# Kernel optimization log

Measured on AMD Instinct MI355X. Metric: run time of the kernel, lower is better.

The kernel has to match this reference:

```python
import jax, jax.numpy as jnp
import numpy as np


def setup_inputs() -> dict:
    key = jax.random.key(0)
    ks = jax.random.split(key, 8)
    B, C, H, W = 4, 128, 64, 64
    C8 = C // 8
    return {
        "x": jax.random.normal(ks[0], (B, C, H, W), dtype=jnp.float32),
        "Wq": jax.random.normal(ks[1], (C8, C), dtype=jnp.float32) * (1.0 / np.sqrt(C)),
        "bq": jax.random.normal(ks[2], (C8,), dtype=jnp.float32) * 0.01,
        "Wk": jax.random.normal(ks[3], (C8, C), dtype=jnp.float32) * (1.0 / np.sqrt(C)),
        "bk": jax.random.normal(ks[4], (C8,), dtype=jnp.float32) * 0.01,
        "Wv": jax.random.normal(ks[5], (C, C), dtype=jnp.float32) * (1.0 / np.sqrt(C)),
        "bv": jax.random.normal(ks[6], (C,), dtype=jnp.float32) * 0.01,
        "gamma": jax.random.normal(ks[7], (1,), dtype=jnp.float32),
    }


def reference(x, Wq, bq, Wk, bk, Wv, bv, gamma):
    B, C, H, W = x.shape
    N = H * W
    xf = x.reshape(B, C, N)  # flatten spatial dims; 1x1 conv == channel matmul
    q = jnp.einsum("oc,bcn->bon", Wq, xf) + bq[None, :, None]  # (B, C8, N)
    k = jnp.einsum("oc,bcn->bon", Wk, xf) + bk[None, :, None]  # (B, C8, N)
    v = jnp.einsum("oc,bcn->bon", Wv, xf) + bv[None, :, None]  # (B, C, N)
    scores = jnp.einsum("bci,bcj->bij", q, k)  # (B, N, N), query rows x key cols
    attn = jax.nn.softmax(scores, axis=-1)
    out = jnp.einsum("bcj,bij->bci", v, attn)  # (B, C, N)
    out = out.reshape(B, C, H, W)
    return gamma[0] * out + x
```

## Files before the change

kernel.cpp:

```cpp
#include <hip/hip_runtime.h>
#include <math.h>

typedef __attribute__((ext_vector_type(8))) short bf16x8;
typedef __attribute__((ext_vector_type(16))) float f32x16;

constexpr int Bn = 4, Cn = 128, C8n = 16, Nn = 4096;

#if __has_builtin(__builtin_amdgcn_exp2f)
#define EXP2F(x) __builtin_amdgcn_exp2f(x)
#else
#define EXP2F(x) exp2f(x)
#endif

__device__ inline unsigned short f2bf(float f) {
    unsigned u = __builtin_bit_cast(unsigned, f);
    u += 0x7fff + ((u >> 16) & 1);
    return (unsigned short)(u >> 16);
}
__device__ inline unsigned pack2(float a, float b) {
    return (unsigned)f2bf(a) | ((unsigned)f2bf(b) << 16);
}
__device__ inline unsigned pkt(float a, float b) {
#if __has_builtin(__builtin_amdgcn_perm)
    return __builtin_amdgcn_perm(__builtin_bit_cast(unsigned, b),
                                 __builtin_bit_cast(unsigned, a), 0x07060302u);
#else
    return (__builtin_bit_cast(unsigned, a) >> 16) |
           (__builtin_bit_cast(unsigned, b) & 0xffff0000u);
#endif
}

__global__ __launch_bounds__(256) void qkv_kernel(
    const float* __restrict__ x,
    const float* __restrict__ Wq, const float* __restrict__ bq,
    const float* __restrict__ Wk, const float* __restrict__ bk,
    const float* __restrict__ Wv, const float* __restrict__ bv,
    unsigned short* __restrict__ qT, unsigned short* __restrict__ kT,
    unsigned short* __restrict__ vsw)
{
    __shared__ unsigned short wlds[160 * 128];
    __shared__ unsigned short v_s[32 * 128];
    __shared__ float qk_s[32][65];
    __shared__ float bfl[160];

    const int tid = threadIdx.x;
    const int b = blockIdx.x >> 6, n0 = (blockIdx.x & 63) << 6;
    const int w = tid >> 6, lane = tid & 63, col = lane & 31, half = lane >> 5;
    const float L2E = 1.4426950408889634f;

    {
        unsigned* wl32 = (unsigned*)wlds;
        for (int i = tid; i < 160 * 32; i += 256) {
            int r = i >> 5, cq = (i & 31) << 2;
            const float* src; float sc = 1.0f;
            if (r < 16)      { src = Wq + (size_t)r * Cn;        sc = L2E; }
            else if (r < 32) { src = Wk + (size_t)(r - 16) * Cn; }
            else             { src = Wv + (size_t)(r - 32) * Cn; }
            float4 t = *reinterpret_cast<const float4*>(&src[cq]);
            int G = cq >> 3;
            unsigned* wp = wl32 + 64 * r + 4 * (G ^ (r & 7)) + ((cq & 7) >> 1);
            wp[0] = pack2(t.x * sc, t.y * sc);
            wp[1] = pack2(t.z * sc, t.w * sc);
        }
        if (tid < 160)
            bfl[tid] = (tid < 16) ? bq[tid] * L2E
                     : (tid < 32) ? bk[tid - 16] : bv[tid - 32];
    }

    const int nx = n0 + ((w & 1) << 5);
    const float* xb = x + ((size_t)b * Cn) * Nn + nx + col;
    bf16x8 af[8];
    #pragma unroll
    for (int s = 0; s < 8; ++s) {
        float v[8];
        #pragma unroll
        for (int j = 0; j < 8; ++j)
            v[j] = xb[(size_t)(16 * s + 8 * half + j) * Nn];
        uint4 u = make_uint4(pack2(v[0], v[1]), pack2(v[2], v[3]),
                             pack2(v[4], v[5]), pack2(v[6], v[7]));
        af[s] = __builtin_bit_cast(bf16x8, u);
    }
    __syncthreads();

    const int mb = (w >> 1) ? 3 : 0;
    const bool three = (w >> 1) == 0;
    f32x16 a0, a1, a2;
    {
        float b0 = bfl[32 * mb + col], b1 = bfl[32 * (mb + 1) + col];
        float b2v = three ? bfl[64 + col] : 0.0f;
        #pragma unroll
        for (int r = 0; r < 16; ++r) { a0[r] = b0; a1[r] = b1; a2[r] = b2v; }
    }
    #pragma unroll
    for (int s = 0; s < 8; ++s) {
        const int off = 8 * ((2 * s + half) ^ (col & 7));
        a0 = __builtin_amdgcn_mfma_f32_32x32x16_bf16(af[s],
             *(const bf16x8*)(wlds + 128 * (32 * mb + col) + off), a0, 0, 0, 0);
        a1 = __builtin_amdgcn_mfma_f32_32x32x16_bf16(af[s],
             *(const bf16x8*)(wlds + 128 * (32 * (mb + 1) + col) + off), a1, 0, 0, 0);
        if (three)
            a2 = __builtin_amdgcn_mfma_f32_32x32x16_bf16(af[s],
                 *(const bf16x8*)(wlds + 128 * (64 + col) + off), a2, 0, 0, 0);
    }

    unsigned* vp32 = (unsigned*)v_s;
    #define VS_WRITE(A) { \
        _Pragma("unroll") for (int g = 0; g < 4; ++g) { \
            int n_ = ((w & 1) << 5) + (g << 3) + (half << 2); \
            int Gn = n_ >> 3; \
            int u_ = 64 * col + 4 * (Gn ^ (col & 7)) + (half << 1); \
            vp32[u_]     = pack2(A[4 * g],     A[4 * g + 1]); \
            vp32[u_ + 1] = pack2(A[4 * g + 2], A[4 * g + 3]); } }

    #define VS_OUT(CT) { \
        int c_ = lane & 31, Gt = ((tid >> 6) << 1) + (lane >> 5); \
        bf16x8 fr = *(const bf16x8*)&v_s[128 * c_ + 8 * (Gt ^ (c_ & 7))]; \
        size_t o_ = ((((size_t)b * 256 + (n0 >> 4) + (tid >> 6)) * 4 + (CT)) * 64 + lane) * 8; \
        *reinterpret_cast<uint4*>(&vsw[o_]) = __builtin_bit_cast(uint4, fr); }

    if (w < 2) {
        #pragma unroll
        for (int r = 0; r < 16; ++r)
            qk_s[col][((w & 1) << 5) + (r & 3) + ((r >> 2) << 3) + (half << 2)] = a0[r];
    } else {
        VS_WRITE(a0)
    }
    __syncthreads();
    VS_OUT(2)
    if (tid < 128) {
        int n = tid & 63, which = tid >> 6;
        unsigned wv_[8];
        #pragma unroll
        for (int i = 0; i < 8; ++i)
            wv_[i] = pack2(qk_s[16 * which + 2 * i][n], qk_s[16 * which + 2 * i + 1][n]);
        unsigned short* dst = (which ? kT : qT) + ((size_t)b * Nn + n0 + n) * C8n;
        *reinterpret_cast<uint4*>(dst)     = make_uint4(wv_[0], wv_[1], wv_[2], wv_[3]);
        *reinterpret_cast<uint4*>(dst + 8) = make_uint4(wv_[4], wv_[5], wv_[6], wv_[7]);
    }
    __syncthreads();
    if (w < 2) VS_WRITE(a1)
    __syncthreads();
    VS_OUT(0)
    __syncthreads();
    if (w >= 2) VS_WRITE(a1)
    __syncthreads();
    VS_OUT(3)
    __syncthreads();
    if (w < 2) VS_WRITE(a2)
    __syncthreads();
    VS_OUT(1)
    #undef VS_WRITE
    #undef VS_OUT
}

__global__ __launch_bounds__(512) void attn_kernel(
    const unsigned short* __restrict__ qT, const unsigned short* __restrict__ kT,
    const unsigned short* __restrict__ vsw, const float* __restrict__ x,
    const float* __restrict__ gamma_p, float* __restrict__ out)
{
    __shared__ unsigned sm_u32[8192];
    __shared__ float ls[2][2][64];
    __shared__ float invl[64];

    const int tid = threadIdx.x, wv = tid >> 6, lane = tid & 63;
    const int col = lane & 31, half = lane >> 5;
    const int xcd = blockIdx.x & 7;
    const int b = xcd >> 1;
    const int q0 = ((((blockIdx.x >> 3) << 1) | (xcd & 1))) << 6;

    const unsigned short* qb = qT + (size_t)b * Nn * C8n;
    bf16x8 qf0 = *(const bf16x8*)&qb[(size_t)(q0 + col) * C8n + 8 * half];
    bf16x8 qf1 = *(const bf16x8*)&qb[(size_t)(q0 + 32 + col) * C8n + 8 * half];

    f32x16 accA[4], accB[4];
    #pragma unroll
    for (int ct = 0; ct < 4; ++ct) { accA[ct] = {}; accB[ct] = {}; }
    float l0 = 0.0f, l1 = 0.0f;
    const unsigned short* kb = kT + (size_t)b * Nn * C8n;

    for (int kt = 0; kt < 16; ++kt) {
        const int j0 = (wv << 9) + (kt << 5);
        const size_t vbase = ((((size_t)b * 256 + (j0 >> 4)) * 4) * 64 + lane) * 8;
        bf16x8 va[4], vb2[4];
        #pragma unroll
        for (int ct = 0; ct < 4; ++ct) {
            va[ct]  = *(const bf16x8*)&vsw[vbase + (size_t)ct * 512];
            vb2[ct] = *(const bf16x8*)&vsw[vbase + (size_t)(4 + ct) * 512];
        }
        bf16x8 kf = *(const bf16x8*)&kb[(size_t)(j0 + col) * C8n + 8 * half];
        f32x16 z = {};
        f32x16 s0 = __builtin_amdgcn_mfma_f32_32x32x16_bf16(kf, qf0, z, 0, 0, 0);
        f32x16 s1 = __builtin_amdgcn_mfma_f32_32x32x16_bf16(kf, qf1, z, 0, 0, 0);

        float p0[16], p1[16];
        float ps0 = 0.0f, ps1 = 0.0f;
        #pragma unroll
        for (int r = 0; r < 16; ++r) { p0[r] = EXP2F(s0[r]); ps0 += p0[r]; }
        #pragma unroll
        for (int r = 0; r < 16; ++r) { p1[r] = EXP2F(s1[r]); ps1 += p1[r]; }
        ps0 += __shfl_xor(ps0, 32); l0 += ps0;
        ps1 += __shfl_xor(ps1, 32); l1 += ps1;

        #define MKPF(P, O, F) { \
            unsigned lo0 = pkt(P[O], P[O + 1]), lo1 = pkt(P[O + 2], P[O + 3]); \
            unsigned hi0 = pkt(P[O + 4], P[O + 5]), hi1 = pkt(P[O + 6], P[O + 7]); \
            unsigned t0 = half ? lo0 : hi0, t1 = half ? lo1 : hi1; \
            unsigned r0 = (unsigned)__shfl_xor((int)t0, 32); \
            unsigned r1 = (unsigned)__shfl_xor((int)t1, 32); \
            uint4 u_ = make_uint4(half ? r0 : lo0, half ? r1 : lo1, \
                                  half ? hi0 : r0, half ? hi1 : r1); \
            F = __builtin_bit_cast(bf16x8, u_); }
        bf16x8 pa0, pa1, pb0, pb1;
        MKPF(p0, 0, pa0) MKPF(p0, 8, pa1)
        MKPF(p1, 0, pb0) MKPF(p1, 8, pb1)
        #undef MKPF

        #pragma unroll
        for (int ct = 0; ct < 4; ++ct) {
            accA[ct] = __builtin_amdgcn_mfma_f32_32x32x16_bf16(va[ct],  pa0, accA[ct], 0, 0, 0);
            accA[ct] = __builtin_amdgcn_mfma_f32_32x32x16_bf16(vb2[ct], pa1, accA[ct], 0, 0, 0);
            accB[ct] = __builtin_amdgcn_mfma_f32_32x32x16_bf16(va[ct],  pb0, accB[ct], 0, 0, 0);
            accB[ct] = __builtin_amdgcn_mfma_f32_32x32x16_bf16(vb2[ct], pb1, accB[ct], 0, 0, 0);
        }
    }

    #define SL_STORE(SL) { \
        ls[SL][0][lane] = l0; ls[SL][1][lane] = l1; \
        unsigned* sb = sm_u32 + (SL) * 4096; \
        _Pragma("unroll") for (int ct = 0; ct < 4; ++ct) \
        _Pragma("unroll") for (int i = 0; i < 8; ++i) { \
            sb[((ct) * 8 + i) * 64 + lane]     = pkt(accA[ct][2 * i], accA[ct][2 * i + 1]); \
            sb[((4 + ct) * 8 + i) * 64 + lane] = pkt(accB[ct][2 * i], accB[ct][2 * i + 1]); } }
    #define SL_ADD(SL) { \
        l0 += ls[SL][0][lane]; l1 += ls[SL][1][lane]; \
        unsigned* sb = sm_u32 + (SL) * 4096; \
        _Pragma("unroll") for (int ct = 0; ct < 4; ++ct) \
        _Pragma("unroll") for (int i = 0; i < 8; ++i) { \
            unsigned ua = sb[((ct) * 8 + i) * 64 + lane]; \
            accA[ct][2 * i]     += __builtin_bit_cast(float, ua << 16); \
            accA[ct][2 * i + 1] += __builtin_bit_cast(float, ua & 0xffff0000u); \
            unsigned ub = sb[((4 + ct) * 8 + i) * 64 + lane]; \
            accB[ct][2 * i]     += __builtin_bit_cast(float, ub << 16); \
            accB[ct][2 * i + 1] += __builtin_bit_cast(float, ub & 0xffff0000u); } }
    #define SL_RMW(SL) { \
        ls[SL][0][lane] += l0; ls[SL][1][lane] += l1; \
        unsigned* sb = sm_u32 + (SL) * 4096; \
        _Pragma("unroll") for (int ct = 0; ct < 4; ++ct) \
        _Pragma("unroll") for (int i = 0; i < 8; ++i) { \
            unsigned ua = sb[((ct) * 8 + i) * 64 + lane]; \
            float x0 = __builtin_bit_cast(float, ua << 16) + accA[ct][2 * i]; \
            float x1 = __builtin_bit_cast(float, ua & 0xffff0000u) + accA[ct][2 * i + 1]; \
            sb[((ct) * 8 + i) * 64 + lane] = pkt(x0, x1); \
            unsigned ub = sb[((4 + ct) * 8 + i) * 64 + lane]; \
            float y0 = __builtin_bit_cast(float, ub << 16) + accB[ct][2 * i]; \
            float y1 = __builtin_bit_cast(float, ub & 0xffff0000u) + accB[ct][2 * i + 1]; \
            sb[((4 + ct) * 8 + i) * 64 + lane] = pkt(y0, y1); } }

    if (wv == 4 || wv == 5) SL_STORE(wv - 4)
    __syncthreads();
    if (wv == 0 || wv == 1) SL_ADD(wv)
    __syncthreads();
    if (wv == 6 || wv == 7) SL_STORE(wv - 6)
    __syncthreads();
    if (wv == 2 || wv == 3) SL_RMW(wv - 2)
    __syncthreads();
    if (wv == 0 || wv == 1) SL_ADD(wv)
    __syncthreads();
    if (wv == 1) SL_STORE(0)
    __syncthreads();
    float* sf = (float*)sm_u32;
    if (wv == 0) {
        SL_ADD(0)
        #pragma unroll
        for (int ct = 0; ct < 4; ++ct)
            #pragma unroll
            for (int r = 0; r < 16; ++r) {
                sf[((ct) * 16 + r) * 64 + lane]     = accA[ct][r];
                sf[((4 + ct) * 16 + r) * 64 + lane] = accB[ct][r];
            }
        if (lane < 32) { invl[col] = 1.0f / l0; invl[32 + col] = 1.0f / l1; }
    }
    __syncthreads();
    #undef SL_STORE
    #undef SL_ADD
    #undef SL_RMW

    {
        const float g = gamma_p[0];
        const int n = tid & 63, ci = tid >> 6;
        const float il = invl[n];
        const int qs = n >> 5, nc = n & 31;
        #pragma unroll
        for (int p = 0; p < 16; ++p) {
            int ch = (p << 3) + ci;
            int ct = ch >> 5, chl = ch & 31;
            int h = (chl >> 2) & 1, r = (chl & 3) | ((chl >> 3) << 2);
            float val = sf[((qs * 4 + ct) * 16 + r) * 64 + nc + (h << 5)];
            size_t idx = ((size_t)(b * Cn + ch)) * Nn + q0 + n;
            out[idx] = g * (val * il) + x[idx];
        }
    }
}

extern "C" void kernel_launch(void* const* d_in, const int* in_sizes, int n_in,
                              void* d_out, int out_size, void* d_ws, size_t ws_size,
                              hipStream_t stream)
{
    const float* x     = (const float*)d_in[0];
    const float* Wq    = (const float*)d_in[1];
    const float* bq    = (const float*)d_in[2];
    const float* Wk    = (const float*)d_in[3];
    const float* bk    = (const float*)d_in[4];
    const float* Wv    = (const float*)d_in[5];
    const float* bv    = (const float*)d_in[6];
    const float* gamma = (const float*)d_in[7];
    float* out = (float*)d_out;

    unsigned short* ws16 = (unsigned short*)d_ws;
    unsigned short* qTw  = ws16;
    unsigned short* kTw  = qTw + (size_t)Bn * Nn * C8n;
    unsigned short* vsww = kTw + (size_t)Bn * Nn * C8n;

    qkv_kernel<<<dim3(256), dim3(256), 0, stream>>>(
        x, Wq, bq, Wk, bk, Wv, bv, qTw, kTw, vsww);

    attn_kernel<<<dim3(256), dim3(512), 0, stream>>>(
        qTw, kTw, vsww, x, gamma, out);
}
```

Baseline: 114.1 us.

## Stage full V tile in LDS once and split attention loop by query half

The QKV kernel now holds the whole 128x64 V tile in shared memory, so all waves write their V fragments at once and then each wave stores one channel tile. This replaces the previous sequence of alternating writes, reads and many block barriers. In the attention kernel the two query halves are processed one after the other inside each key step, which shortens the live range of the score and probability arrays and is meant to lower register pressure. The loop is also marked not to unroll. The larger V buffer raises LDS use in the QKV kernel, and the sequential halves may leave less room to overlap MFMA with exp work.

Result: no change. 113.8 us (-0.2%).

```diff
diff --git a/kernel.cpp b/kernel.cpp
--- a/kernel.cpp
+++ b/kernel.cpp
@@ -39,7 +39,7 @@
     unsigned short* __restrict__ vsw)
 {
     __shared__ unsigned short wlds[160 * 128];
-    __shared__ unsigned short v_s[32 * 128];
+    __shared__ unsigned short v_s[128 * 64];
     __shared__ float qk_s[32][65];
     __shared__ float bfl[160];
 
@@ -104,29 +104,27 @@
     }
 
     unsigned* vp32 = (unsigned*)v_s;
-    #define VS_WRITE(A) { \
+    #define VS_WRITE(A, C0) { \
+        const int c_ = (C0) + col; \
         _Pragma("unroll") for (int g = 0; g < 4; ++g) { \
-            int n_ = ((w & 1) << 5) + (g << 3) + (half << 2); \
-            int Gn = n_ >> 3; \
-            int u_ = 64 * col + 4 * (Gn ^ (col & 7)) + (half << 1); \
-            vp32[u_]     = pack2(A[4 * g],     A[4 * g + 1]); \
-            vp32[u_ + 1] = pack2(A[4 * g + 2], A[4 * g + 3]); } }
-
-    #define VS_OUT(CT) { \
-        int c_ = lane & 31, Gt = ((tid >> 6) << 1) + (lane >> 5); \
-        bf16x8 fr = *(const bf16x8*)&v_s[128 * c_ + 8 * (Gt ^ (c_ & 7))]; \
-        size_t o_ = ((((size_t)b * 256 + (n0 >> 4) + (tid >> 6)) * 4 + (CT)) * 64 + lane) * 8; \
-        *reinterpret_cast<uint4*>(&vsw[o_]) = __builtin_bit_cast(uint4, fr); }
+            int Gn = ((w & 1) << 2) + g; \
+            unsigned* up = vp32 + 32 * c_ + 4 * (Gn ^ (c_ & 7)) + (half << 1); \
+            up[0] = pack2(A[4 * g],     A[4 * g + 1]); \
+            up[1] = pack2(A[4 * g + 2], A[4 * g + 3]); } }
 
     if (w < 2) {
         #pragma unroll
         for (int r = 0; r < 16; ++r)
             qk_s[col][((w & 1) << 5) + (r & 3) + ((r >> 2) << 3) + (half << 2)] = a0[r];
+        VS_WRITE(a1, 0)
+        VS_WRITE(a2, 32)
     } else {
-        VS_WRITE(a0)
-    }
-    __syncthreads();
-    VS_OUT(2)
+        VS_WRITE(a0, 64)
+        VS_WRITE(a1, 96)
+    }
+    #undef VS_WRITE
+    __syncthreads();
+
     if (tid < 128) {
         int n = tid & 63, which = tid >> 6;
         unsigned wv_[8];
@@ -137,20 +135,16 @@
         *reinterpret_cast<uint4*>(dst)     = make_uint4(wv_[0], wv_[1], wv_[2], wv_[3]);
         *reinterpret_cast<uint4*>(dst + 8) = make_uint4(wv_[4], wv_[5], wv_[6], wv_[7]);
     }
-    __syncthreads();
-    if (w < 2) VS_WRITE(a1)
-    __syncthreads();
-    VS_OUT(0)
-    __syncthreads();
-    if (w >= 2) VS_WRITE(a1)
-    __syncthreads();
-    VS_OUT(3)
-    __syncthreads();
-    if (w < 2) VS_WRITE(a2)
-    __syncthreads();
-    VS_OUT(1)
-    #undef VS_WRITE
-    #undef VS_OUT
+    {
+        const int ct = w, c_ = (ct << 5) + col;
+        #pragma unroll
+        for (int t = 0; t < 4; ++t) {
+            int Gn = (t << 1) + half;
+            bf16x8 fr = *(const bf16x8*)(vp32 + 32 * c_ + 4 * (Gn ^ (c_ & 7)));
+            size_t o_ = ((((size_t)b * 256 + (n0 >> 4) + t) * 4 + ct) * 64 + lane) * 8;
+            *reinterpret_cast<uint4*>(&vsw[o_]) = __builtin_bit_cast(uint4, fr);
+        }
+    }
 }
 
 __global__ __launch_bounds__(512) void attn_kernel(
@@ -178,6 +172,17 @@
     float l0 = 0.0f, l1 = 0.0f;
     const unsigned short* kb = kT + (size_t)b * Nn * C8n;
 
+    #define MKPF(P, O, F) { \
+        unsigned lo0 = pkt(P[O], P[O + 1]), lo1 = pkt(P[O + 2], P[O + 3]); \
+        unsigned hi0 = pkt(P[O + 4], P[O + 5]), hi1 = pkt(P[O + 6], P[O + 7]); \
+        unsigned t0 = half ? lo0 : hi0, t1 = half ? lo1 : hi1; \
+        unsigned r0 = (unsigned)__shfl_xor((int)t0, 32); \
+        unsigned r1 = (unsigned)__shfl_xor((int)t1, 32); \
+        uint4 u_ = make_uint4(half ? r0 : lo0, half ? r1 : lo1, \
+                              half ? hi0 : r0, half ? hi1 : r1); \
+        F = __builtin_bit_cast(bf16x8, u_); }
+
+    #pragma unroll 1
     for (int kt = 0; kt < 16; ++kt) {
         const int j0 = (wv << 9) + (kt << 5);
         const size_t vbase = ((((size_t)b * 256 + (j0 >> 4)) * 4) * 64 + lane) * 8;
@@ -189,40 +194,37 @@
         }
         bf16x8 kf = *(const bf16x8*)&kb[(size_t)(j0 + col) * C8n + 8 * half];
         f32x16 z = {};
-        f32x16 s0 = __builtin_amdgcn_mfma_f32_32x32x16_bf16(kf, qf0, z, 0, 0, 0);
-        f32x16 s1 = __builtin_amdgcn_mfma_f32_32x32x16_bf16(kf, qf1, z, 0, 0, 0);
-
-        float p0[16], p1[16];
-        float ps0 = 0.0f, ps1 = 0.0f;
-        #pragma unroll
-        for (int r = 0; r < 16; ++r) { p0[r] = EXP2F(s0[r]); ps0 += p0[r]; }
-        #pragma unroll
-        for (int r = 0; r < 16; ++r) { p1[r] = EXP2F(s1[r]); ps1 += p1[r]; }
-        ps0 += __shfl_xor(ps0, 32); l0 += ps0;
-        ps1 += __shfl_xor(ps1, 32); l1 += ps1;
-
-        #define MKPF(P, O, F) { \
-            unsigned lo0 = pkt(P[O], P[O + 1]), lo1 = pkt(P[O + 2], P[O + 3]); \
-            unsigned hi0 = pkt(P[O + 4], P[O + 5]), hi1 = pkt(P[O + 6], P[O + 7]); \
-            unsigned t0 = half ? lo0 : hi0, t1 = half ? lo1 : hi1; \
-            unsigned r0 = (unsigned)__shfl_xor((int)t0, 32); \
-            unsigned r1 = (unsigned)__shfl_xor((int)t1, 32); \
-            uint4 u_ = make_uint4(half ? r0 : lo0, half ? r1 : lo1, \
-                                  half ? hi0 : r0, half ? hi1 : r1); \
-            F = __builtin_bit_cast(bf16x8, u_); }
-        bf16x8 pa0, pa1, pb0, pb1;
-        MKPF(p0, 0, pa0) MKPF(p0, 8, pa1)
-        MKPF(p1, 0, pb0) MKPF(p1, 8, pb1)
-        #undef MKPF
-
-        #pragma unroll
-        for (int ct = 0; ct < 4; ++ct) {
-            accA[ct] = __builtin_amdgcn_mfma_f32_32x32x16_bf16(va[ct],  pa0, accA[ct], 0, 0, 0);
-            accA[ct] = __builtin_amdgcn_mfma_f32_32x32x16_bf16(vb2[ct], pa1, accA[ct], 0, 0, 0);
-            accB[ct] = __builtin_amdgcn_mfma_f32_32x32x16_bf16(va[ct],  pb0, accB[ct], 0, 0, 0);
-            accB[ct] = __builtin_amdgcn_mfma_f32_32x32x16_bf16(vb2[ct], pb1, accB[ct], 0, 0, 0);
-        }
-    }
+
+        {
+            f32x16 s = __builtin_amdgcn_mfma_f32_32x32x16_bf16(kf, qf0, z, 0, 0, 0);
+            float p[16]; float ps = 0.0f;
+            #pragma unroll
+            for (int r = 0; r < 16; ++r) { p[r] = EXP2F(s[r]); ps += p[r]; }
+            ps += __shfl_xor(ps, 32); l0 += ps;
+            bf16x8 pf0, pf1;
+            MKPF(p, 0, pf0) MKPF(p, 8, pf1)
+            #pragma unroll
+            for (int ct = 0; ct < 4; ++ct) {
+                accA[ct] = __builtin_amdgcn_mfma_f32_32x32x16_bf16(va[ct],  pf0, accA[ct], 0, 0, 0);
+                accA[ct] = __builtin_amdgcn_mfma_f32_32x32x16_bf16(vb2[ct], pf1, accA[ct], 0, 0, 0);
+            }
+        }
+        {
+            f32x16 s = __builtin_amdgcn_mfma_f32_32x32x16_bf16(kf, qf1, z, 0, 0, 0);
+            float p[16]; float ps = 0.0f;
+            #pragma unroll
+            for (int r = 0; r < 16; ++r) { p[r] = EXP2F(s[r]); ps += p[r]; }
+            ps += __shfl_xor(ps, 32); l1 += ps;
+            bf16x8 pf0, pf1;
+            MKPF(p, 0, pf0) MKPF(p, 8, pf1)
+            #pragma unroll
+            for (int ct = 0; ct < 4; ++ct) {
+                accB[ct] = __builtin_amdgcn_mfma_f32_32x32x16_bf16(va[ct],  pf0, accB[ct], 0, 0, 0);
+                accB[ct] = __builtin_amdgcn_mfma_f32_32x32x16_bf16(vb2[ct], pf1, accB[ct], 0, 0, 0);
+            }
+        }
+    }
+    #undef MKPF
 
     #define SL_STORE(SL) { \
         ls[SL][0][lane] = l0; ls[SL][1][lane] = l1; \
```
